# Kernel tuning notes

Hardware: AMD Instinct MI355X
Metric: run time of the kernel (lower is better)

The kernel has to match this reference:

```python
import jax, jax.numpy as jnp
import numpy as np

KERNEL_MUL = [2.0, 2.0]
KERNEL_NUM = [5, 1]
FIX_SIGMA = [None, 1.68]


def setup_inputs() -> dict:
    key = jax.random.key(0)
    k0, k1, k2, k3 = jax.random.split(key, 4)
    B, D0, D1 = 4096, 2048, 128
    return {
        "src_f0": jax.random.normal(k0, (B, D0), dtype=jnp.float32),
        "src_f1": jax.random.normal(k1, (B, D1), dtype=jnp.float32),
        "tar_f0": jax.random.normal(k2, (B, D0), dtype=jnp.float32),
        "tar_f1": jax.random.normal(k3, (B, D1), dtype=jnp.float32),
    }


def _gaussian_kernel(src, tar, kernel_mul, kernel_num, fix_sigma):
    n_samples = src.shape[0] + tar.shape[0]
    total = jnp.concatenate([src, tar], axis=0)  # [2B, D]
    # pairwise squared L2 distance without the O(N^2*D) expanded intermediate
    sq = jnp.sum(total * total, axis=1)
    l2 = sq[:, None] + sq[None, :] - 2.0 * (total @ total.T)  # [2B, 2B]
    if fix_sigma:
        bandwidth = jnp.asarray(fix_sigma, dtype=l2.dtype)
    else:
        # original uses L2_distance.data (detached) for the bandwidth estimate
        bandwidth = jax.lax.stop_gradient(jnp.sum(l2)) / (n_samples ** 2 - n_samples)
    bandwidth = bandwidth / (kernel_mul ** (kernel_num // 2))
    kernel = jnp.zeros_like(l2)
    for i in range(kernel_num):
        kernel = kernel + jnp.exp(-l2 / (bandwidth * kernel_mul ** i))
    return kernel


def reference(src_f0, src_f1, tar_f0, tar_f1):
    src_list = [src_f0, src_f1]
    tar_list = [tar_f0, tar_f1]
    joint = None
    for i in range(len(src_list)):
        k = _gaussian_kernel(src_list[i], tar_list[i], KERNEL_MUL[i], KERNEL_NUM[i], FIX_SIGMA[i])
        joint = k if joint is None else joint * k
    B = src_f0.shape[0]
    XX = joint[:B, :B]
    YY = joint[B:, B:]
    XY = joint[:B, B:]
    YX = joint[B:, :B]
    return jnp.mean(XX + YY - XY - YX)
```

## Files before the change

kernel.cpp:

```cpp
#include <hip/hip_runtime.h>
#include <stdint.h>

#define B_ROWS 4096
#define NTOT   8192
#define D0     2048
#define D1     128
#define TAU    80.0f

#define OFF_ACC   0
#define OFF_S0    8
#define OFF_BW    16
#define OFF_CNT   20
#define OFF_DONE  24
#define OFF_M0    32
#define OFF_SQ1   8320
#define OFF_T1    41216
#define OFF_CAND  2138368
#define ZERO_WORDS 2056

typedef float f32x4 __attribute__((ext_vector_type(4)));
typedef long i64;

#define LDST 136

__global__ void p0a(const float* __restrict__ src1, const float* __restrict__ tar1, char* __restrict__ ws) {
    if (blockIdx.x == 0) {
        unsigned* w = (unsigned*)ws;
        for (int i = threadIdx.x; i < ZERO_WORDS; i += 256) w[i] = 0;
    }
    int wave = threadIdx.x >> 6, lane = threadIdx.x & 63;
    int row = blockIdx.x * 4 + wave;
    const float2* rp = (const float2*)(row < B_ROWS ? src1 + (size_t)row * D1
                                                    : tar1 + (size_t)(row - B_ROWS) * D1);
    float2 v = rp[lane];
    float sq = v.x * v.x + v.y * v.y;
    #pragma unroll
    for (int off = 32; off; off >>= 1) sq += __shfl_down(sq, off);
    if (lane == 0) ((float*)(ws + OFF_SQ1))[row] = sq;
    int pk = __builtin_amdgcn_cvt_pk_fp8_f32(v.x, v.y, 0, false);
    __builtin_nontemporal_store((unsigned short)(pk & 0xffff),
        (unsigned short*)(ws + OFF_T1 + (size_t)row * 128 + lane * 2));
}

__global__ __launch_bounds__(256, 4) void phaseA(char* __restrict__ ws, unsigned cap) {
    int tid = blockIdx.x;
    int bi = (int)((129.0 - sqrt(129.0 * 129.0 - 8.0 * (double)tid)) * 0.5);
    while (((bi + 1) * (129 - (bi + 1))) / 2 <= tid) bi++;
    while ((bi * (129 - bi)) / 2 > tid) bi--;
    int bj = bi + (tid - (bi * (129 - bi)) / 2);

    __shared__ __align__(16) unsigned char At[128 * LDST];
    __shared__ __align__(16) unsigned char Bt[128 * LDST];
    const uint4* t1 = (const uint4*)(ws + OFF_T1);
    int t = threadIdx.x;
    int lane = t & 63, wave = t >> 6;
    int wm = wave & 1, wn = wave >> 1;
    int quad = lane >> 4;
    int Abase = bi * 128, Bbase = bj * 128;

    #pragma unroll
    for (int i = 0; i < 4; i++) {
        int q = t + 256 * i;
        int r = q >> 3, c = q & 7;
        uint4 va = t1[(size_t)(Abase + r) * 8 + c];
        *(uint4*)(At + r * LDST + c * 16) = va;
        uint4 vb = t1[(size_t)(Bbase + r) * 8 + c];
        *(uint4*)(Bt + r * LDST + c * 16) = vb;
    }
    __syncthreads();

    f32x4 acc[4][4];
    #pragma unroll
    for (int i = 0; i < 4; i++)
        #pragma unroll
        for (int j = 0; j < 4; j++) acc[i][j] = (f32x4){0.f, 0.f, 0.f, 0.f};

    #pragma unroll
    for (int ks = 0; ks < 4; ks++) {
        int koff = ks * 32 + quad * 8;
        i64 af[4], bf[4];
        #pragma unroll
        for (int mi = 0; mi < 4; mi++) {
            int row = wm * 64 + mi * 16 + (lane & 15);
            af[mi] = *(const i64*)(At + row * LDST + koff);
        }
        #pragma unroll
        for (int nj = 0; nj < 4; nj++) {
            int row = wn * 64 + nj * 16 + (lane & 15);
            bf[nj] = *(const i64*)(Bt + row * LDST + koff);
        }
        #pragma unroll
        for (int mi = 0; mi < 4; mi++)
            #pragma unroll
            for (int nj = 0; nj < 4; nj++)
                acc[mi][nj] = __builtin_amdgcn_mfma_f32_16x16x32_fp8_fp8(
                    af[mi], bf[nj], acc[mi][nj], 0, 0, 0);
    }

    const float* sq1 = (const float*)(ws + OFF_SQ1);
    unsigned* cnt = (unsigned*)(ws + OFF_CNT);
    uint2* cand = (uint2*)(ws + OFF_CAND);
    f32x4 sqa[4];
    #pragma unroll
    for (int mi = 0; mi < 4; mi++)
        sqa[mi] = *(const f32x4*)&sq1[Abase + wm * 64 + mi * 16 + quad * 4];
    #pragma unroll
    for (int nj = 0; nj < 4; nj++) {
        int b = Bbase + wn * 64 + nj * 16 + (lane & 15);
        float sqb = sq1[b];
        #pragma unroll
        for (int mi = 0; mi < 4; mi++) {
            int abase = Abase + wm * 64 + mi * 16 + quad * 4;
            #pragma unroll
            for (int r = 0; r < 4; r++) {
                int a = abase + r;
                float l2 = sqa[mi][r] + sqb - 2.0f * acc[mi][nj][r];
                if (l2 < TAU && a < b) {
                    unsigned idx = atomicAdd(cnt, 1u);
                    if (idx < cap) cand[idx] = make_uint2((unsigned)a, (unsigned)b);
                }
            }
        }
    }
}

__global__ void bwk1(const float* __restrict__ src0, const float* __restrict__ tar0, char* __restrict__ ws) {
    if (*(volatile unsigned*)(ws + OFF_CNT) == 0) return;
    int d4 = blockIdx.x * 256 + threadIdx.x;
    int rbase = blockIdx.y * 64;
    const float4* base = (const float4*)(rbase < B_ROWS ? src0 + (size_t)rbase * D0
                                                        : tar0 + (size_t)(rbase - B_ROWS) * D0);
    float4 cs = {0.f, 0.f, 0.f, 0.f};
    float sq = 0.f;
    for (int r = 0; r < 64; r++) {
        float4 v = base[(size_t)r * 512 + d4];
        cs.x += v.x; cs.y += v.y; cs.z += v.z; cs.w += v.w;
        sq += v.x * v.x + v.y * v.y + v.z * v.z + v.w * v.w;
    }
    float* m0 = (float*)(ws + OFF_M0);
    atomicAdd(&m0[d4 * 4 + 0], cs.x);
    atomicAdd(&m0[d4 * 4 + 1], cs.y);
    atomicAdd(&m0[d4 * 4 + 2], cs.z);
    atomicAdd(&m0[d4 * 4 + 3], cs.w);
    #pragma unroll
    for (int off = 32; off; off >>= 1) sq += __shfl_down(sq, off);
    __shared__ float red[4];
    int lane = threadIdx.x & 63, wave = threadIdx.x >> 6;
    if (lane == 0) red[wave] = sq;
    __syncthreads();
    if (threadIdx.x == 0)
        atomicAdd((double*)(ws + OFF_S0), (double)(red[0] + red[1] + red[2] + red[3]));
}

__global__ void phaseB(const float* __restrict__ src0, const float* __restrict__ src1,
                       const float* __restrict__ tar0, const float* __restrict__ tar1,
                       char* __restrict__ ws, unsigned cap, float* __restrict__ out) {
    __shared__ double red[4];
    __shared__ float fred[4];
    __shared__ float bws;
    unsigned cnt = *(const unsigned*)(ws + OFF_CNT);
    if (cnt > cap) cnt = cap;
    int lane = threadIdx.x & 63, wave = threadIdx.x >> 6;
    if (cnt > 0) {
        const float* m0 = (const float*)(ws + OFF_M0);
        float s = 0.f;
        for (int j = threadIdx.x; j < 2048; j += 256) { float v = m0[j]; s += v * v; }
        #pragma unroll
        for (int off = 32; off; off >>= 1) s += __shfl_down(s, off);
        if (lane == 0) fred[wave] = s;
        __syncthreads();
        if (threadIdx.x == 0) {
            double m2 = (double)fred[0] + fred[1] + fred[2] + fred[3];
            double S0 = *(double*)(ws + OFF_S0);
            double lsum2 = 2.0 * (double)NTOT * S0 - 2.0 * m2;
            bws = (float)(lsum2 / ((double)NTOT * NTOT - NTOT) / 4.0);
        }
        __syncthreads();
        float bw = bws;
        const uint2* cand = (const uint2*)(ws + OFF_CAND);
        unsigned gw = blockIdx.x * 4 + wave;
        unsigned nw = gridDim.x * 4;
        double lsum = 0.0;
        for (unsigned i = gw; i < cnt; i += nw) {
            uint2 p = cand[i];
            unsigned a = p.x, b = p.y;
            const float* ra0 = a < B_ROWS ? src0 + (size_t)a * D0 : tar0 + (size_t)(a - B_ROWS) * D0;
            const float* rb0 = b < B_ROWS ? src0 + (size_t)b * D0 : tar0 + (size_t)(b - B_ROWS) * D0;
            const float* ra1 = a < B_ROWS ? src1 + (size_t)a * D1 : tar1 + (size_t)(a - B_ROWS) * D1;
            const float* rb1 = b < B_ROWS ? src1 + (size_t)b * D1 : tar1 + (size_t)(b - B_ROWS) * D1;
            float d1;
            {
                float2 x = ((const float2*)ra1)[lane];
                float2 y = ((const float2*)rb1)[lane];
                float dx = x.x - y.x, dy = x.y - y.y;
                d1 = dx * dx + dy * dy;
            }
            float d0 = 0.f;
            #pragma unroll
            for (int j = 0; j < 8; j++) {
                float4 x = ((const float4*)ra0)[lane + 64 * j];
                float4 y = ((const float4*)rb0)[lane + 64 * j];
                float dx = x.x - y.x, dy = x.y - y.y, dz = x.z - y.z, dw = x.w - y.w;
                d0 += dx * dx + dy * dy + dz * dz + dw * dw;
            }
            #pragma unroll
            for (int off = 32; off; off >>= 1) {
                d0 += __shfl_down(d0, off);
                d1 += __shfl_down(d1, off);
            }
            if (lane == 0) {
                float k1 = expf(-d1 / 1.68f);
                float k0 = 0.f, bwj = bw;
                #pragma unroll
                for (int j = 0; j < 5; j++) { k0 += expf(-d0 / bwj); bwj *= 2.0f; }
                float sgn = ((a < B_ROWS) == (b < B_ROWS)) ? 1.0f : -1.0f;
                lsum += (double)(2.0f * sgn * k0 * k1);
            }
        }
        if (lane == 0) red[wave] = lsum;
        __syncthreads();
        if (threadIdx.x == 0)
            atomicAdd((double*)(ws + OFF_ACC), red[0] + red[1] + red[2] + red[3]);
    }
    __threadfence();
    if (threadIdx.x == 0) {
        unsigned d = atomicAdd((unsigned*)(ws + OFF_DONE), 1u);
        if (d == gridDim.x - 1) {
            double acc = atomicAdd((double*)(ws + OFF_ACC), 0.0);
            out[0] = (float)((acc + (double)NTOT * 5.0) / ((double)B_ROWS * (double)B_ROWS));
        }
    }
}

extern "C" void kernel_launch(void* const* d_in, const int* in_sizes, int n_in,
                              void* d_out, int out_size, void* d_ws, size_t ws_size,
                              hipStream_t stream) {
    const float* src0 = (const float*)d_in[0];
    const float* src1 = (const float*)d_in[1];
    const float* tar0 = (const float*)d_in[2];
    const float* tar1 = (const float*)d_in[3];
    char* ws = (char*)d_ws;
    unsigned cap = 0;
    if (ws_size > (size_t)OFF_CAND + 8) {
        size_t c = (ws_size - OFF_CAND) / 8;
        if (c > (size_t)4 * 1024 * 1024) c = (size_t)4 * 1024 * 1024;
        cap = (unsigned)c;
    }
    p0a<<<2048, 256, 0, stream>>>(src1, tar1, ws);
    phaseA<<<2080, 256, 0, stream>>>(ws, cap);
    bwk1<<<dim3(2, 128), 256, 0, stream>>>(src0, tar0, ws);
    phaseB<<<64, 256, 0, stream>>>(src0, src1, tar0, tar1, ws, cap, (float*)d_out);
}
```

Before: 117.8 us.

## Enlarge phaseA tiles to 256x256, fuse bandwidth reduction into phaseB

phaseA now uses 256x256 triangle tiles with 512-thread blocks, so there are fewer blocks and each one reuses more staged data. The separate bwk1 reduction kernel is removed. Its column-sum and sum-of-squares work now runs at the start of phaseB, across all 64 blocks, followed by a spin-wait grid barrier on a workspace counter. p0a switches to nontemporal loads. The barrier assumes all 64 blocks are co-resident and adds a spin cost. Each phaseB block now streams 128 rows of the 2048-wide features, which may lengthen phaseB.

```diff
diff --git a/kernel.cpp b/kernel.cpp
--- a/kernel.cpp
+++ b/kernel.cpp
@@ -9,7 +9,7 @@
 
 #define OFF_ACC   0
 #define OFF_S0    8
-#define OFF_BW    16
+#define OFF_MDONE 16
 #define OFF_CNT   20
 #define OFF_DONE  24
 #define OFF_M0    32
@@ -19,6 +19,7 @@
 #define ZERO_WORDS 2056
 
 typedef float f32x4 __attribute__((ext_vector_type(4)));
+typedef float f32x2 __attribute__((ext_vector_type(2)));
 typedef long i64;
 
 #define LDST 136
@@ -30,9 +31,9 @@
     }
     int wave = threadIdx.x >> 6, lane = threadIdx.x & 63;
     int row = blockIdx.x * 4 + wave;
-    const float2* rp = (const float2*)(row < B_ROWS ? src1 + (size_t)row * D1
-                                                    : tar1 + (size_t)(row - B_ROWS) * D1);
-    float2 v = rp[lane];
+    const f32x2* rp = (const f32x2*)(row < B_ROWS ? src1 + (size_t)row * D1
+                                                  : tar1 + (size_t)(row - B_ROWS) * D1);
+    f32x2 v = __builtin_nontemporal_load(&rp[lane]);
     float sq = v.x * v.x + v.y * v.y;
     #pragma unroll
     for (int off = 32; off; off >>= 1) sq += __shfl_down(sq, off);
@@ -42,25 +43,25 @@
         (unsigned short*)(ws + OFF_T1 + (size_t)row * 128 + lane * 2));
 }
 
-__global__ __launch_bounds__(256, 4) void phaseA(char* __restrict__ ws, unsigned cap) {
+__global__ __launch_bounds__(512, 2) void phaseA(char* __restrict__ ws, unsigned cap) {
     int tid = blockIdx.x;
-    int bi = (int)((129.0 - sqrt(129.0 * 129.0 - 8.0 * (double)tid)) * 0.5);
-    while (((bi + 1) * (129 - (bi + 1))) / 2 <= tid) bi++;
-    while ((bi * (129 - bi)) / 2 > tid) bi--;
-    int bj = bi + (tid - (bi * (129 - bi)) / 2);
-
-    __shared__ __align__(16) unsigned char At[128 * LDST];
-    __shared__ __align__(16) unsigned char Bt[128 * LDST];
+    int bi = (int)((65.0 - sqrt(65.0 * 65.0 - 8.0 * (double)tid)) * 0.5);
+    while (((bi + 1) * (65 - (bi + 1))) / 2 <= tid) bi++;
+    while ((bi * (65 - bi)) / 2 > tid) bi--;
+    int bj = bi + (tid - (bi * (65 - bi)) / 2);
+
+    __shared__ __align__(16) unsigned char At[256 * LDST];
+    __shared__ __align__(16) unsigned char Bt[256 * LDST];
     const uint4* t1 = (const uint4*)(ws + OFF_T1);
     int t = threadIdx.x;
     int lane = t & 63, wave = t >> 6;
     int wm = wave & 1, wn = wave >> 1;
     int quad = lane >> 4;
-    int Abase = bi * 128, Bbase = bj * 128;
+    int Abase = bi * 256, Bbase = bj * 256;
 
     #pragma unroll
     for (int i = 0; i < 4; i++) {
-        int q = t + 256 * i;
+        int q = t + 512 * i;
         int r = q >> 3, c = q & 7;
         uint4 va = t1[(size_t)(Abase + r) * 8 + c];
         *(uint4*)(At + r * LDST + c * 16) = va;
@@ -69,19 +70,19 @@
     }
     __syncthreads();
 
-    f32x4 acc[4][4];
-    #pragma unroll
-    for (int i = 0; i < 4; i++)
+    f32x4 acc[8][4];
+    #pragma unroll
+    for (int i = 0; i < 8; i++)
         #pragma unroll
         for (int j = 0; j < 4; j++) acc[i][j] = (f32x4){0.f, 0.f, 0.f, 0.f};
 
     #pragma unroll
     for (int ks = 0; ks < 4; ks++) {
         int koff = ks * 32 + quad * 8;
-        i64 af[4], bf[4];
-        #pragma unroll
-        for (int mi = 0; mi < 4; mi++) {
-            int row = wm * 64 + mi * 16 + (lane & 15);
+        i64 af[8], bf[4];
+        #pragma unroll
+        for (int mi = 0; mi < 8; mi++) {
+            int row = wm * 128 + mi * 16 + (lane & 15);
             af[mi] = *(const i64*)(At + row * LDST + koff);
         }
         #pragma unroll
@@ -90,7 +91,7 @@
             bf[nj] = *(const i64*)(Bt + row * LDST + koff);
         }
         #pragma unroll
-        for (int mi = 0; mi < 4; mi++)
+        for (int mi = 0; mi < 8; mi++)
             #pragma unroll
             for (int nj = 0; nj < 4; nj++)
                 acc[mi][nj] = __builtin_amdgcn_mfma_f32_16x16x32_fp8_fp8(
@@ -100,17 +101,17 @@
     const float* sq1 = (const float*)(ws + OFF_SQ1);
     unsigned* cnt = (unsigned*)(ws + OFF_CNT);
     uint2* cand = (uint2*)(ws + OFF_CAND);
-    f32x4 sqa[4];
-    #pragma unroll
-    for (int mi = 0; mi < 4; mi++)
-        sqa[mi] = *(const f32x4*)&sq1[Abase + wm * 64 + mi * 16 + quad * 4];
+    f32x4 sqa[8];
+    #pragma unroll
+    for (int mi = 0; mi < 8; mi++)
+        sqa[mi] = *(const f32x4*)&sq1[Abase + wm * 128 + mi * 16 + quad * 4];
     #pragma unroll
     for (int nj = 0; nj < 4; nj++) {
         int b = Bbase + wn * 64 + nj * 16 + (lane & 15);
         float sqb = sq1[b];
         #pragma unroll
-        for (int mi = 0; mi < 4; mi++) {
-            int abase = Abase + wm * 64 + mi * 16 + quad * 4;
+        for (int mi = 0; mi < 8; mi++) {
+            int abase = Abase + wm * 128 + mi * 16 + quad * 4;
             #pragma unroll
             for (int r = 0; r < 4; r++) {
                 int a = abase + r;
@@ -122,34 +123,6 @@
             }
         }
     }
-}
-
-__global__ void bwk1(const float* __restrict__ src0, const float* __restrict__ tar0, char* __restrict__ ws) {
-    if (*(volatile unsigned*)(ws + OFF_CNT) == 0) return;
-    int d4 = blockIdx.x * 256 + threadIdx.x;
-    int rbase = blockIdx.y * 64;
-    const float4* base = (const float4*)(rbase < B_ROWS ? src0 + (size_t)rbase * D0
-                                                        : tar0 + (size_t)(rbase - B_ROWS) * D0);
-    float4 cs = {0.f, 0.f, 0.f, 0.f};
-    float sq = 0.f;
-    for (int r = 0; r < 64; r++) {
-        float4 v = base[(size_t)r * 512 + d4];
-        cs.x += v.x; cs.y += v.y; cs.z += v.z; cs.w += v.w;
-        sq += v.x * v.x + v.y * v.y + v.z * v.z + v.w * v.w;
-    }
-    float* m0 = (float*)(ws + OFF_M0);
-    atomicAdd(&m0[d4 * 4 + 0], cs.x);
-    atomicAdd(&m0[d4 * 4 + 1], cs.y);
-    atomicAdd(&m0[d4 * 4 + 2], cs.z);
-    atomicAdd(&m0[d4 * 4 + 3], cs.w);
-    #pragma unroll
-    for (int off = 32; off; off >>= 1) sq += __shfl_down(sq, off);
-    __shared__ float red[4];
-    int lane = threadIdx.x & 63, wave = threadIdx.x >> 6;
-    if (lane == 0) red[wave] = sq;
-    __syncthreads();
-    if (threadIdx.x == 0)
-        atomicAdd((double*)(ws + OFF_S0), (double)(red[0] + red[1] + red[2] + red[3]));
 }
 
 __global__ void phaseB(const float* __restrict__ src0, const float* __restrict__ src1,
@@ -162,6 +135,40 @@
     if (cnt > cap) cnt = cap;
     int lane = threadIdx.x & 63, wave = threadIdx.x >> 6;
     if (cnt > 0) {
+        {
+            int rbase = blockIdx.x * 128;
+            const float4* base = (const float4*)(rbase < B_ROWS ? src0 + (size_t)rbase * D0
+                                                                : tar0 + (size_t)(rbase - B_ROWS) * D0);
+            float* m0 = (float*)(ws + OFF_M0);
+            float sq = 0.f;
+            #pragma unroll
+            for (int h = 0; h < 2; h++) {
+                int d4 = threadIdx.x + h * 256;
+                float4 cs = {0.f, 0.f, 0.f, 0.f};
+                for (int r = 0; r < 128; r++) {
+                    float4 v = base[(size_t)r * 512 + d4];
+                    cs.x += v.x; cs.y += v.y; cs.z += v.z; cs.w += v.w;
+                    sq += v.x * v.x + v.y * v.y + v.z * v.z + v.w * v.w;
+                }
+                atomicAdd(&m0[d4 * 4 + 0], cs.x);
+                atomicAdd(&m0[d4 * 4 + 1], cs.y);
+                atomicAdd(&m0[d4 * 4 + 2], cs.z);
+                atomicAdd(&m0[d4 * 4 + 3], cs.w);
+            }
+            #pragma unroll
+            for (int off = 32; off; off >>= 1) sq += __shfl_down(sq, off);
+            if (lane == 0) fred[wave] = sq;
+            __syncthreads();
+            if (threadIdx.x == 0) {
+                atomicAdd((double*)(ws + OFF_S0),
+                          (double)(fred[0] + fred[1] + fred[2] + fred[3]));
+                __threadfence();
+                atomicAdd((unsigned*)(ws + OFF_MDONE), 1u);
+                while (*(volatile unsigned*)(ws + OFF_MDONE) < 64u) { }
+            }
+            __syncthreads();
+            __threadfence();
+        }
         const float* m0 = (const float*)(ws + OFF_M0);
         float s = 0.f;
         for (int j = threadIdx.x; j < 2048; j += 256) { float v = m0[j]; s += v * v; }
@@ -247,7 +254,6 @@
         cap = (unsigned)c;
     }
     p0a<<<2048, 256, 0, stream>>>(src1, tar1, ws);
-    phaseA<<<2080, 256, 0, stream>>>(ws, cap);
-    bwk1<<<dim3(2, 128), 256, 0, stream>>>(src0, tar0, ws);
+    phaseA<<<528, 512, 0, stream>>>(ws, cap);
     phaseB<<<64, 256, 0, stream>>>(src0, src1, tar0, tar1, ws, cap, (float*)d_out);
 }
```

Result: slower. 122.0 us (+3.6%).
